# Performance work log

Measured on AMD Instinct MI355X. Metric: run time of the kernel, lower is better.

## Reference

```python
import jax, jax.numpy as jnp
import numpy as np

N_PRED, N_DRIFT, N_DW, N_NODES = 12, 2, 3, 4096
B = 128
L = N_PRED + 2 * N_DRIFT  # 16


def setup_inputs() -> dict:
    key = jax.random.key(0)
    ks = jax.random.split(key, 8)
    inp = jax.random.normal(ks[0], (B, N_NODES, N_DW, L), jnp.float32)
    ctrl = jax.random.normal(ks[1], (B, N_NODES, N_PRED), jnp.float32)
    # learned offsets (init zeros in torch; randomized here so interpolation is non-trivial)
    offset_t = jax.random.normal(ks[2], (N_DW, N_PRED), jnp.float32) * 0.5
    offset_n = jax.random.normal(ks[3], (N_DW, N_PRED), jnp.float32) * 0.5
    conv_t_w = jax.random.normal(ks[4], (1, N_DW, 3), jnp.float32) / np.sqrt(N_DW * 3)
    conv_t_b = jnp.zeros((1,), jnp.float32)
    conv_n_w = jax.random.normal(ks[5], (N_PRED, N_PRED, N_DW), jnp.float32) / np.sqrt(N_PRED * N_DW)
    conv_n_b = jnp.zeros((N_PRED,), jnp.float32)
    W = jax.random.normal(ks[6], (N_PRED, N_PRED), jnp.float32)
    bparam = jax.random.normal(ks[7], (N_NODES, N_PRED), jnp.float32)
    return dict(inp=inp, ctrl=ctrl, offset_t=offset_t, offset_n=offset_n,
                conv_t_w=conv_t_w, conv_t_b=conv_t_b, conv_n_w=conv_n_w,
                conv_n_b=conv_n_b, W=W, bparam=bparam)


def _deform(x, offset):
    # x: [BN, n_d_w, L]; offset: [n_d_w, n_pred]
    pos_add = (jnp.arange(N_PRED, dtype=jnp.float32) + N_DRIFT)[None, :]  # [1, n_pred]
    pos = jnp.tanh(offset) * N_DRIFT + pos_add                           # [d, p], in [j, j+2*drift)
    key_f = jnp.floor(pos)            # torch int(pos); pos >= 0 so floor == trunc
    frac = pos - key_f                # gradient flows to offset only through frac
    idx = key_f.astype(jnp.int32)     # [d, p]
    rows = jnp.arange(N_DW)[:, None]  # [d, 1]
    v0 = x[:, rows, idx]              # [BN, d, p]
    v1 = x[:, rows, idx + 1]
    return v0 * (1.0 - frac) + v1 * frac


def reference(inp, ctrl, offset_t, offset_n, conv_t_w, conv_t_b, conv_n_w, conv_n_b, W, bparam):
    b, n = inp.shape[0], inp.shape[1]
    x = inp.reshape(b * n, N_DW, L)
    # the written slice [n_drift:-n_drift] is exactly the interpolated region
    dt = _deform(x, offset_t)  # [BN, n_d_w, n_pred]
    dn = _deform(x, offset_n)  # [BN, n_d_w, n_pred]
    # temporal branch: Conv1d(n_d_w -> 1, k=3, pad=1)
    pred_t = jax.lax.conv_general_dilated(
        dt, conv_t_w, window_strides=(1,), padding=[(1, 1)],
        dimension_numbers=('NCH', 'OIH', 'NCH'))
    pred_t = (pred_t + conv_t_b[None, :, None]).reshape(b, n, N_PRED)
    # node branch: Conv1d(n_pred -> n_pred, k=n_d_w) over permuted [BN, n_pred, n_d_w]
    # == full contraction: out[b,o] = sum_{c,k} w[o,c,k] * dn[b,k,c]
    pred_n = (jnp.einsum('bkc,ock->bo', dn, conv_n_w) + conv_n_b).reshape(b, n, N_PRED)
    gate = jax.nn.sigmoid(jnp.einsum('bnp,pq->bnq', ctrl, W) + bparam)
    return pred_n * gate + pred_t * (1.0 - gate)
```

## Files before the change

### kernel.cpp

```cpp
#include <hip/hip_runtime.h>
#include <math.h>

#define N_PRED  12
#define N_DRIFT 2
#define N_DW    3
#define N_NODES 4096
#define BB      128
#define LL      16
#define BN      (BB * N_NODES)

__global__ void deform_precompute(const float* __restrict__ offset_t,
                                  const float* __restrict__ offset_n,
                                  const float* __restrict__ conv_t_w,
                                  const float* __restrict__ conv_n_w,
                                  float* __restrict__ Mt,
                                  float* __restrict__ Mn) {
    int t = threadIdx.x;
    if (t >= N_PRED * N_DW * LL) return;
    int q  = t % N_PRED;
    int kl = t / N_PRED;
    int k  = kl / LL;
    int l  = kl % LL;

    auto coef = [&](const float* off, int c) -> float {
        float pos = tanhf(off[k * N_PRED + c]) * (float)N_DRIFT
                    + (float)(c + N_DRIFT);
        float idf = floorf(pos);
        float fr  = pos - idf;
        int   id  = (int)idf;
        if (l == id)     return 1.0f - fr;
        if (l == id + 1) return fr;
        return 0.0f;
    };

    float mt = 0.0f;
    #pragma unroll
    for (int h = 0; h < 3; ++h) {
        int c = q - 1 + h;
        if (c < 0 || c >= N_PRED) continue;
        mt += conv_t_w[k * 3 + h] * coef(offset_t, c);
    }

    float mn = 0.0f;
    #pragma unroll
    for (int c = 0; c < N_PRED; ++c) {
        mn += conv_n_w[q * (N_PRED * N_DW) + c * N_DW + k] * coef(offset_n, c);
    }

    Mt[kl * N_PRED + q] = mt;
    Mn[kl * N_PRED + q] = mn;
}

__global__ __launch_bounds__(256) void deform_main(
        const float* __restrict__ inp,
        const float* __restrict__ ctrl,
        const float* __restrict__ W,
        const float* __restrict__ bparam,
        const float* __restrict__ conv_t_b,
        const float* __restrict__ conv_n_b,
        const float* __restrict__ Mt,
        const float* __restrict__ Mn,
        float* __restrict__ out) {
    int tid = blockIdx.x * 256 + threadIdx.x;
    int n   = tid & (N_NODES - 1);

    float x[48];
    const float4* xp = (const float4*)(inp + (size_t)tid * 48);
    #pragma unroll
    for (int i = 0; i < 12; ++i) {
        float4 v = xp[i];
        x[4 * i + 0] = v.x; x[4 * i + 1] = v.y;
        x[4 * i + 2] = v.z; x[4 * i + 3] = v.w;
    }

    float c[12];
    const float4* cp = (const float4*)(ctrl + (size_t)tid * N_PRED);
    #pragma unroll
    for (int i = 0; i < 3; ++i) {
        float4 v = cp[i];
        c[4 * i + 0] = v.x; c[4 * i + 1] = v.y;
        c[4 * i + 2] = v.z; c[4 * i + 3] = v.w;
    }

    float accg[12];
    const float4* bp = (const float4*)(bparam + (size_t)n * N_PRED);
    #pragma unroll
    for (int i = 0; i < 3; ++i) {
        float4 v = bp[i];
        accg[4 * i + 0] = v.x; accg[4 * i + 1] = v.y;
        accg[4 * i + 2] = v.z; accg[4 * i + 3] = v.w;
    }

    float acct[12], accn[12];
    float ctb = conv_t_b[0];
    #pragma unroll
    for (int q = 0; q < N_PRED; ++q) {
        acct[q] = ctb;
        accn[q] = conv_n_b[q];
    }

    #pragma unroll
    for (int kl = 0; kl < 48; ++kl) {
        float xv = x[kl];
        #pragma unroll
        for (int q = 0; q < N_PRED; ++q) {
            acct[q] = fmaf(Mt[kl * N_PRED + q], xv, acct[q]);
            accn[q] = fmaf(Mn[kl * N_PRED + q], xv, accn[q]);
        }
    }

    #pragma unroll
    for (int p = 0; p < N_PRED; ++p) {
        float cv = c[p];
        #pragma unroll
        for (int q = 0; q < N_PRED; ++q) {
            accg[q] = fmaf(cv, W[p * N_PRED + q], accg[q]);
        }
    }

    float4 o4[3];
    float* ov = (float*)o4;
    #pragma unroll
    for (int q = 0; q < N_PRED; ++q) {
        float g = 1.0f / (1.0f + __expf(-accg[q]));
        ov[q] = accn[q] * g + acct[q] * (1.0f - g);
    }
    float4* op = (float4*)(out + (size_t)tid * N_PRED);
    op[0] = o4[0]; op[1] = o4[1]; op[2] = o4[2];
}

extern "C" void kernel_launch(void* const* d_in, const int* in_sizes, int n_in,
                              void* d_out, int out_size, void* d_ws, size_t ws_size,
                              hipStream_t stream) {
    const float* inp      = (const float*)d_in[0];
    const float* ctrl     = (const float*)d_in[1];
    const float* offset_t = (const float*)d_in[2];
    const float* offset_n = (const float*)d_in[3];
    const float* conv_t_w = (const float*)d_in[4];
    const float* conv_t_b = (const float*)d_in[5];
    const float* conv_n_w = (const float*)d_in[6];
    const float* conv_n_b = (const float*)d_in[7];
    const float* W        = (const float*)d_in[8];
    const float* bparam   = (const float*)d_in[9];
    float* out = (float*)d_out;

    float* Mt = (float*)d_ws;
    float* Mn = Mt + N_DW * LL * N_PRED;

    deform_precompute<<<1, 576, 0, stream>>>(offset_t, offset_n,
                                             conv_t_w, conv_n_w, Mt, Mn);
    deform_main<<<BN / 256, 256, 0, stream>>>(inp, ctrl, W, bparam,
                                              conv_t_b, conv_n_b, Mt, Mn, out);
}
```

Baseline: 203.4 us.

## Stage input, ctrl and output through shared memory for coalesced global access

Each block cooperatively loads its slice of inp and ctrl with contiguous float4 loads into LDS (inp padded to 13 float4 per row to avoid bank conflicts). Each thread then reads its own row from LDS. Outputs are written back through LDS so the global stores are contiguous. Block size drops from 256 to 128 threads. This targets strided per-thread global access, at the cost of extra LDS traffic, barriers and about 32KB of LDS per block, which may limit occupancy.

```diff
diff --git a/kernel.cpp b/kernel.cpp
--- a/kernel.cpp
+++ b/kernel.cpp
@@ -8,6 +8,9 @@
 #define BB      128
 #define LL      16
 #define BN      (BB * N_NODES)
+#define TPB     128
+#define NBLK    (BN / TPB)
+#define XROW    13
 
 __global__ void deform_precompute(const float* __restrict__ offset_t,
                                   const float* __restrict__ offset_n,
@@ -51,7 +54,7 @@
     Mn[kl * N_PRED + q] = mn;
 }
 
-__global__ __launch_bounds__(256) void deform_main(
+__global__ __launch_bounds__(TPB) void deform_main(
         const float* __restrict__ inp,
         const float* __restrict__ ctrl,
         const float* __restrict__ W,
@@ -61,34 +64,52 @@
         const float* __restrict__ Mt,
         const float* __restrict__ Mn,
         float* __restrict__ out) {
-    int tid = blockIdx.x * 256 + threadIdx.x;
-    int n   = tid & (N_NODES - 1);
+    __shared__ float4 xs4[TPB * XROW];
+    __shared__ float4 cs4[TPB * 3];
+
+    const int t   = threadIdx.x;
+    const int tid = blockIdx.x * TPB + t;
+    const int n   = tid & (N_NODES - 1);
+
+    const float4* gin = (const float4*)inp + (size_t)blockIdx.x * (TPB * 12);
+    #pragma unroll
+    for (int i = 0; i < 12; ++i) {
+        int A = i * TPB + t;
+        float4 v = gin[A];
+        xs4[(A / 12) * XROW + (A % 12)] = v;
+    }
+    const float4* gct = (const float4*)ctrl + (size_t)blockIdx.x * (TPB * 3);
+    #pragma unroll
+    for (int i = 0; i < 3; ++i) {
+        int A = i * TPB + t;
+        cs4[A] = gct[A];
+    }
+    __syncthreads();
 
     float x[48];
-    const float4* xp = (const float4*)(inp + (size_t)tid * 48);
     #pragma unroll
-    for (int i = 0; i < 12; ++i) {
-        float4 v = xp[i];
-        x[4 * i + 0] = v.x; x[4 * i + 1] = v.y;
-        x[4 * i + 2] = v.z; x[4 * i + 3] = v.w;
+    for (int c = 0; c < 12; ++c) {
+        float4 v = xs4[t * XROW + c];
+        x[4 * c + 0] = v.x; x[4 * c + 1] = v.y;
+        x[4 * c + 2] = v.z; x[4 * c + 3] = v.w;
     }
-
-    float c[12];
-    const float4* cp = (const float4*)(ctrl + (size_t)tid * N_PRED);
+    float cr[12];
     #pragma unroll
     for (int i = 0; i < 3; ++i) {
-        float4 v = cp[i];
-        c[4 * i + 0] = v.x; c[4 * i + 1] = v.y;
-        c[4 * i + 2] = v.z; c[4 * i + 3] = v.w;
+        float4 v = cs4[t * 3 + i];
+        cr[4 * i + 0] = v.x; cr[4 * i + 1] = v.y;
+        cr[4 * i + 2] = v.z; cr[4 * i + 3] = v.w;
     }
 
     float accg[12];
-    const float4* bp = (const float4*)(bparam + (size_t)n * N_PRED);
-    #pragma unroll
-    for (int i = 0; i < 3; ++i) {
-        float4 v = bp[i];
-        accg[4 * i + 0] = v.x; accg[4 * i + 1] = v.y;
-        accg[4 * i + 2] = v.z; accg[4 * i + 3] = v.w;
+    {
+        const float* bp = bparam + (size_t)n * N_PRED;
+        #pragma unroll
+        for (int i = 0; i < 3; ++i) {
+            float4 v = *(const float4*)(bp + 4 * i);
+            accg[4 * i + 0] = v.x; accg[4 * i + 1] = v.y;
+            accg[4 * i + 2] = v.z; accg[4 * i + 3] = v.w;
+        }
     }
 
     float acct[12], accn[12];
@@ -111,7 +132,7 @@
 
     #pragma unroll
     for (int p = 0; p < N_PRED; ++p) {
-        float cv = c[p];
+        float cv = cr[p];
         #pragma unroll
         for (int q = 0; q < N_PRED; ++q) {
             accg[q] = fmaf(cv, W[p * N_PRED + q], accg[q]);
@@ -125,8 +146,19 @@
         float g = 1.0f / (1.0f + __expf(-accg[q]));
         ov[q] = accn[q] * g + acct[q] * (1.0f - g);
     }
-    float4* op = (float4*)(out + (size_t)tid * N_PRED);
-    op[0] = o4[0]; op[1] = o4[1]; op[2] = o4[2];
+
+    __syncthreads();
+    #pragma unroll
+    for (int j = 0; j < 3; ++j) {
+        xs4[t * 3 + j] = o4[j];
+    }
+    __syncthreads();
+    float4* gout = (float4*)out + (size_t)blockIdx.x * (TPB * 3);
+    #pragma unroll
+    for (int j = 0; j < 3; ++j) {
+        int A = j * TPB + t;
+        gout[A] = xs4[A];
+    }
 }
 
 extern "C" void kernel_launch(void* const* d_in, const int* in_sizes, int n_in,
@@ -149,6 +181,6 @@
 
     deform_precompute<<<1, 576, 0, stream>>>(offset_t, offset_n,
                                              conv_t_w, conv_n_w, Mt, Mn);
-    deform_main<<<BN / 256, 256, 0, stream>>>(inp, ctrl, W, bparam,
-                                              conv_t_b, conv_n_b, Mt, Mn, out);
+    deform_main<<<NBLK, TPB, 0, stream>>>(inp, ctrl, W, bparam,
+                                          conv_t_b, conv_n_b, Mt, Mn, out);
 }
```

Result: no change. 202.7 us (-0.4%).

## Process four points per thread to reuse interleaved weight loads

Applied to the files above, without the earlier changes.

Each thread now handles four points, so every precomputed weight value loaded is applied to four inputs instead of one. The two weight tables are interleaved into one array so both branches read from the same row. Inputs are streamed in chunks of twelve to bound live registers. Holding 96 accumulators per thread raises register pressure and lowers occupancy, which may hurt latency hiding on a memory-heavy kernel.

```diff
diff --git a/kernel.cpp b/kernel.cpp
--- a/kernel.cpp
+++ b/kernel.cpp
@@ -8,13 +8,16 @@
 #define BB      128
 #define LL      16
 #define BN      (BB * N_NODES)
+#define TPB     256
+#define G       4
+#define PPB     (TPB * G)
+#define NBLK    (BN / PPB)
 
 __global__ void deform_precompute(const float* __restrict__ offset_t,
                                   const float* __restrict__ offset_n,
                                   const float* __restrict__ conv_t_w,
                                   const float* __restrict__ conv_n_w,
-                                  float* __restrict__ Mt,
-                                  float* __restrict__ Mn) {
+                                  float* __restrict__ M) {
     int t = threadIdx.x;
     if (t >= N_PRED * N_DW * LL) return;
     int q  = t % N_PRED;
@@ -47,86 +50,110 @@
         mn += conv_n_w[q * (N_PRED * N_DW) + c * N_DW + k] * coef(offset_n, c);
     }
 
-    Mt[kl * N_PRED + q] = mt;
-    Mn[kl * N_PRED + q] = mn;
+    M[kl * 24 + q]      = mt;
+    M[kl * 24 + 12 + q] = mn;
 }
 
-__global__ __launch_bounds__(256) void deform_main(
+__global__ __launch_bounds__(TPB, 2) void deform_main(
         const float* __restrict__ inp,
         const float* __restrict__ ctrl,
         const float* __restrict__ W,
         const float* __restrict__ bparam,
         const float* __restrict__ conv_t_b,
         const float* __restrict__ conv_n_b,
-        const float* __restrict__ Mt,
-        const float* __restrict__ Mn,
+        const float* __restrict__ M,
         float* __restrict__ out) {
-    int tid = blockIdx.x * 256 + threadIdx.x;
-    int n   = tid & (N_NODES - 1);
+    const int t    = threadIdx.x;
+    const int base = blockIdx.x * PPB;
 
-    float x[48];
-    const float4* xp = (const float4*)(inp + (size_t)tid * 48);
+    int p[G];
     #pragma unroll
-    for (int i = 0; i < 12; ++i) {
-        float4 v = xp[i];
-        x[4 * i + 0] = v.x; x[4 * i + 1] = v.y;
-        x[4 * i + 2] = v.z; x[4 * i + 3] = v.w;
+    for (int j = 0; j < G; ++j) p[j] = base + j * TPB + t;
+
+    float acct[G][N_PRED], accn[G][N_PRED];
+    {
+        float ctb = conv_t_b[0];
+        #pragma unroll
+        for (int q = 0; q < N_PRED; ++q) {
+            float cnb = conv_n_b[q];
+            #pragma unroll
+            for (int j = 0; j < G; ++j) {
+                acct[j][q] = ctb;
+                accn[j][q] = cnb;
+            }
+        }
     }
 
-    float c[12];
-    const float4* cp = (const float4*)(ctrl + (size_t)tid * N_PRED);
-    #pragma unroll
-    for (int i = 0; i < 3; ++i) {
-        float4 v = cp[i];
-        c[4 * i + 0] = v.x; c[4 * i + 1] = v.y;
-        c[4 * i + 2] = v.z; c[4 * i + 3] = v.w;
-    }
-
-    float accg[12];
-    const float4* bp = (const float4*)(bparam + (size_t)n * N_PRED);
-    #pragma unroll
-    for (int i = 0; i < 3; ++i) {
-        float4 v = bp[i];
-        accg[4 * i + 0] = v.x; accg[4 * i + 1] = v.y;
-        accg[4 * i + 2] = v.z; accg[4 * i + 3] = v.w;
-    }
-
-    float acct[12], accn[12];
-    float ctb = conv_t_b[0];
-    #pragma unroll
-    for (int q = 0; q < N_PRED; ++q) {
-        acct[q] = ctb;
-        accn[q] = conv_n_b[q];
-    }
-
-    #pragma unroll
-    for (int kl = 0; kl < 48; ++kl) {
-        float xv = x[kl];
+    #pragma unroll 1
+    for (int c = 0; c < 4; ++c) {
+        float4 xc[G][3];
         #pragma unroll
-        for (int q = 0; q < N_PRED; ++q) {
-            acct[q] = fmaf(Mt[kl * N_PRED + q], xv, acct[q]);
-            accn[q] = fmaf(Mn[kl * N_PRED + q], xv, accn[q]);
+        for (int j = 0; j < G; ++j) {
+            const float4* xp = (const float4*)(inp + (size_t)p[j] * 48) + c * 3;
+            #pragma unroll
+            for (int i = 0; i < 3; ++i) xc[j][i] = xp[i];
+        }
+        const float* Mc = M + c * 12 * 24;
+        #pragma unroll
+        for (int kk = 0; kk < 12; ++kk) {
+            float xv[G];
+            #pragma unroll
+            for (int j = 0; j < G; ++j)
+                xv[j] = ((const float*)xc[j])[kk];
+            #pragma unroll
+            for (int q = 0; q < N_PRED; ++q) {
+                float wt = Mc[kk * 24 + q];
+                float wn = Mc[kk * 24 + 12 + q];
+                #pragma unroll
+                for (int j = 0; j < G; ++j) {
+                    acct[j][q] = fmaf(wt, xv[j], acct[j][q]);
+                    accn[j][q] = fmaf(wn, xv[j], accn[j][q]);
+                }
+            }
         }
     }
 
     #pragma unroll
-    for (int p = 0; p < N_PRED; ++p) {
-        float cv = c[p];
+    for (int j = 0; j < G; ++j) {
+        const int n = p[j] & (N_NODES - 1);
+
+        float cr[N_PRED];
+        const float4* cp = (const float4*)(ctrl + (size_t)p[j] * N_PRED);
+        #pragma unroll
+        for (int i = 0; i < 3; ++i) {
+            float4 v = cp[i];
+            cr[4 * i + 0] = v.x; cr[4 * i + 1] = v.y;
+            cr[4 * i + 2] = v.z; cr[4 * i + 3] = v.w;
+        }
+
+        float accg[N_PRED];
+        const float4* bp = (const float4*)(bparam + (size_t)n * N_PRED);
+        #pragma unroll
+        for (int i = 0; i < 3; ++i) {
+            float4 v = bp[i];
+            accg[4 * i + 0] = v.x; accg[4 * i + 1] = v.y;
+            accg[4 * i + 2] = v.z; accg[4 * i + 3] = v.w;
+        }
+
+        #pragma unroll
+        for (int pp = 0; pp < N_PRED; ++pp) {
+            float cv = cr[pp];
+            #pragma unroll
+            for (int q = 0; q < N_PRED; ++q) {
+                accg[q] = fmaf(cv, W[pp * N_PRED + q], accg[q]);
+            }
+        }
+
+        float4 o4[3];
+        float* ov = (float*)o4;
         #pragma unroll
         for (int q = 0; q < N_PRED; ++q) {
-            accg[q] = fmaf(cv, W[p * N_PRED + q], accg[q]);
+            float g = 1.0f / (1.0f + __expf(-accg[q]));
+            ov[q] = accn[j][q] * g + acct[j][q] * (1.0f - g);
         }
+        float4* op = (float4*)(out + (size_t)p[j] * N_PRED);
+        op[0] = o4[0]; op[1] = o4[1]; op[2] = o4[2];
     }
-
-    float4 o4[3];
-    float* ov = (float*)o4;
-    #pragma unroll
-    for (int q = 0; q < N_PRED; ++q) {
-        float g = 1.0f / (1.0f + __expf(-accg[q]));
-        ov[q] = accn[q] * g + acct[q] * (1.0f - g);
-    }
-    float4* op = (float4*)(out + (size_t)tid * N_PRED);
-    op[0] = o4[0]; op[1] = o4[1]; op[2] = o4[2];
 }
 
 extern "C" void kernel_launch(void* const* d_in, const int* in_sizes, int n_in,
@@ -144,11 +171,10 @@
     const float* bparam   = (const float*)d_in[9];
     float* out = (float*)d_out;
 
-    float* Mt = (float*)d_ws;
-    float* Mn = Mt + N_DW * LL * N_PRED;
+    float* M = (float*)d_ws;
 
     deform_precompute<<<1, 576, 0, stream>>>(offset_t, offset_n,
-                                             conv_t_w, conv_n_w, Mt, Mn);
-    deform_main<<<BN / 256, 256, 0, stream>>>(inp, ctrl, W, bparam,
-                                              conv_t_b, conv_n_b, Mt, Mn, out);
+                                             conv_t_w, conv_n_w, M);
+    deform_main<<<NBLK, TPB, 0, stream>>>(inp, ctrl, W, bparam,
+                                          conv_t_b, conv_n_b, M, out);
 }
```

New measurement: 225.9 us. +11.1%, slower.

## Fold all linear maps into one bf16x3 MFMA GEMM with packed weights

Applied to the files above, without the earlier changes.

Packs the deform/conv matrices, gate weight W and biases into a single 64x48 matrix, split into bf16 hi/lo parts in a precompute kernel. The main kernel then computes temporal, node and gate pre-activations with split-bf16 16x16x32 MFMA instructions per 16-row tile, replacing per-thread scalar FMA loops. This removes the scalar FMA cost and changes memory access to lane-cooperative row loads. It trades this for conversion work, masked scalar stores and a small precision loss from the three-term bf16 split.

```diff
diff --git a/kernel.cpp b/kernel.cpp
--- a/kernel.cpp
+++ b/kernel.cpp
@@ -6,24 +6,37 @@
 #define N_DW    3
 #define N_NODES 4096
 #define BB      128
-#define LL      16
 #define BN      (BB * N_NODES)
+#define NTILES  (BN / 16)
+#define RPW     4
+#define WPB     4
+#define NBLK    (NTILES / (RPW * WPB))
+
+typedef __attribute__((ext_vector_type(8))) short bf16x8;
+typedef __attribute__((ext_vector_type(4))) float f32x4;
+
+static __device__ __forceinline__ unsigned short bf16_rne(float f) {
+    unsigned int u = __float_as_uint(f);
+    u = (u + 0x7FFFu + ((u >> 16) & 1u)) >> 16;
+    return (unsigned short)u;
+}
+static __device__ __forceinline__ float bf16_to_f32(unsigned short h) {
+    return __uint_as_float(((unsigned int)h) << 16);
+}
 
 __global__ void deform_precompute(const float* __restrict__ offset_t,
                                   const float* __restrict__ offset_n,
                                   const float* __restrict__ conv_t_w,
+                                  const float* __restrict__ conv_t_b,
                                   const float* __restrict__ conv_n_w,
-                                  float* __restrict__ Mt,
-                                  float* __restrict__ Mn) {
-    int t = threadIdx.x;
-    if (t >= N_PRED * N_DW * LL) return;
-    int q  = t % N_PRED;
-    int kl = t / N_PRED;
-    int k  = kl / LL;
-    int l  = kl % LL;
-
-    auto coef = [&](const float* off, int c) -> float {
-        float pos = tanhf(off[k * N_PRED + c]) * (float)N_DRIFT
+                                  const float* __restrict__ conv_n_b,
+                                  const float* __restrict__ W,
+                                  unsigned short* __restrict__ wsB) {
+    __shared__ float Ms[64][48];
+    const int t = threadIdx.x;
+
+    auto coef = [&](const float* off, int kw, int c, int l) -> float {
+        float pos = tanhf(off[kw * N_PRED + c]) * (float)N_DRIFT
                     + (float)(c + N_DRIFT);
         float idf = floorf(pos);
         float fr  = pos - idf;
@@ -33,100 +46,140 @@
         return 0.0f;
     };
 
-    float mt = 0.0f;
-    #pragma unroll
-    for (int h = 0; h < 3; ++h) {
-        int c = q - 1 + h;
-        if (c < 0 || c >= N_PRED) continue;
-        mt += conv_t_w[k * 3 + h] * coef(offset_t, c);
-    }
-
-    float mn = 0.0f;
-    #pragma unroll
-    for (int c = 0; c < N_PRED; ++c) {
-        mn += conv_n_w[q * (N_PRED * N_DW) + c * N_DW + k] * coef(offset_n, c);
-    }
-
-    Mt[kl * N_PRED + q] = mt;
-    Mn[kl * N_PRED + q] = mn;
+    for (int e = t; e < 64 * 48; e += 256) {
+        int k = e / 48, col = e % 48;
+        float v = 0.0f;
+        if (k < 48) {
+            int kw = k >> 4, l = k & 15;
+            if (col < 12) {
+                #pragma unroll
+                for (int h = 0; h < 3; ++h) {
+                    int c = col - 1 + h;
+                    if (c < 0 || c >= N_PRED) continue;
+                    v += conv_t_w[kw * 3 + h] * coef(offset_t, kw, c, l);
+                }
+            } else if (col >= 16 && col < 28) {
+                int q = col - 16;
+                for (int c = 0; c < N_PRED; ++c)
+                    v += conv_n_w[q * (N_PRED * N_DW) + c * N_DW + kw]
+                         * coef(offset_n, kw, c, l);
+            }
+        } else if (k < 60) {
+            if (col >= 32 && col < 44) v = W[(k - 48) * N_PRED + (col - 32)];
+        } else if (k == 60) {
+            if (col < 12)                 v = conv_t_b[0];
+            else if (col >= 16 && col < 28) v = conv_n_b[col - 16];
+        }
+        Ms[k][col] = v;
+    }
+    __syncthreads();
+
+    for (int e = t; e < 3 * 2 * 64 * 8; e += 256) {
+        int j    = e & 7;
+        int lane = (e >> 3) & 63;
+        int kh   = (e >> 9) & 1;
+        int ct   = e >> 10;
+        int k    = kh * 32 + ((lane >> 4) << 3) + j;
+        int col  = (lane & 15) + 16 * ct;
+        float v  = Ms[k][col];
+        unsigned short hi = bf16_rne(v);
+        unsigned short lo = bf16_rne(v - bf16_to_f32(hi));
+        int off_hi = ((ct * 2 + kh) * 2) * 512 + lane * 8 + j;
+        wsB[off_hi]       = hi;
+        wsB[off_hi + 512] = lo;
+    }
 }
 
 __global__ __launch_bounds__(256) void deform_main(
         const float* __restrict__ inp,
         const float* __restrict__ ctrl,
-        const float* __restrict__ W,
         const float* __restrict__ bparam,
-        const float* __restrict__ conv_t_b,
-        const float* __restrict__ conv_n_b,
-        const float* __restrict__ Mt,
-        const float* __restrict__ Mn,
+        const unsigned short* __restrict__ wsB,
         float* __restrict__ out) {
-    int tid = blockIdx.x * 256 + threadIdx.x;
-    int n   = tid & (N_NODES - 1);
-
-    float x[48];
-    const float4* xp = (const float4*)(inp + (size_t)tid * 48);
+    const int lane = threadIdx.x & 63;
+    const int wid  = blockIdx.x * WPB + (threadIdx.x >> 6);
+    const int quad = lane >> 4;
+    const int col  = lane & 15;
+
+    bf16x8 Bh[3][2], Bl[3][2];
     #pragma unroll
-    for (int i = 0; i < 12; ++i) {
-        float4 v = xp[i];
-        x[4 * i + 0] = v.x; x[4 * i + 1] = v.y;
-        x[4 * i + 2] = v.z; x[4 * i + 3] = v.w;
-    }
-
-    float c[12];
-    const float4* cp = (const float4*)(ctrl + (size_t)tid * N_PRED);
-    #pragma unroll
-    for (int i = 0; i < 3; ++i) {
-        float4 v = cp[i];
-        c[4 * i + 0] = v.x; c[4 * i + 1] = v.y;
-        c[4 * i + 2] = v.z; c[4 * i + 3] = v.w;
-    }
-
-    float accg[12];
-    const float4* bp = (const float4*)(bparam + (size_t)n * N_PRED);
-    #pragma unroll
-    for (int i = 0; i < 3; ++i) {
-        float4 v = bp[i];
-        accg[4 * i + 0] = v.x; accg[4 * i + 1] = v.y;
-        accg[4 * i + 2] = v.z; accg[4 * i + 3] = v.w;
-    }
-
-    float acct[12], accn[12];
-    float ctb = conv_t_b[0];
-    #pragma unroll
-    for (int q = 0; q < N_PRED; ++q) {
-        acct[q] = ctb;
-        accn[q] = conv_n_b[q];
-    }
-
-    #pragma unroll
-    for (int kl = 0; kl < 48; ++kl) {
-        float xv = x[kl];
+    for (int ct = 0; ct < 3; ++ct) {
         #pragma unroll
-        for (int q = 0; q < N_PRED; ++q) {
-            acct[q] = fmaf(Mt[kl * N_PRED + q], xv, acct[q]);
-            accn[q] = fmaf(Mn[kl * N_PRED + q], xv, accn[q]);
-        }
-    }
-
-    #pragma unroll
-    for (int p = 0; p < N_PRED; ++p) {
-        float cv = c[p];
+        for (int kh = 0; kh < 2; ++kh) {
+            const bf16x8* ph =
+                (const bf16x8*)(wsB + ((ct * 2 + kh) * 2) * 512);
+            Bh[ct][kh] = ph[lane];
+            Bl[ct][kh] = ph[lane + 64];
+        }
+    }
+
+    const bool active = (col < 12);
+    const int  bcol   = active ? col : 11;
+
+    #pragma unroll 1
+    for (int r = 0; r < RPW; ++r) {
+        const int rt        = wid * RPW + r;
+        const int base_pair = rt * 16;
+        const int pair      = base_pair + col;
+
+        const float4* xp =
+            (const float4*)(inp + (size_t)pair * 48 + quad * 8);
+        float4 a0 = xp[0], a1 = xp[1];
+
+        const float* bbase;
+        if (quad < 2)      bbase = inp  + (size_t)pair * 48 + 32 + quad * 8;
+        else if (quad == 2) bbase = ctrl + (size_t)pair * 12;
+        else               bbase = ctrl + (size_t)pair * 12 + 8;
+        float4 b0 = *(const float4*)bbase;
+        float4 b1;
+        if (quad == 3) b1 = make_float4(1.0f, 0.0f, 0.0f, 0.0f);
+        else           b1 = *((const float4*)bbase + 1);
+
+        float za[8] = {a0.x, a0.y, a0.z, a0.w, a1.x, a1.y, a1.z, a1.w};
+        float zb[8] = {b0.x, b0.y, b0.z, b0.w, b1.x, b1.y, b1.z, b1.w};
+        union { bf16x8 v; unsigned short u[8]; } Ah0, Al0, Ah1, Al1;
         #pragma unroll
-        for (int q = 0; q < N_PRED; ++q) {
-            accg[q] = fmaf(cv, W[p * N_PRED + q], accg[q]);
-        }
-    }
-
-    float4 o4[3];
-    float* ov = (float*)o4;
-    #pragma unroll
-    for (int q = 0; q < N_PRED; ++q) {
-        float g = 1.0f / (1.0f + __expf(-accg[q]));
-        ov[q] = accn[q] * g + acct[q] * (1.0f - g);
-    }
-    float4* op = (float4*)(out + (size_t)tid * N_PRED);
-    op[0] = o4[0]; op[1] = o4[1]; op[2] = o4[2];
+        for (int j = 0; j < 8; ++j) {
+            unsigned short h0 = bf16_rne(za[j]);
+            Ah0.u[j] = h0;
+            Al0.u[j] = bf16_rne(za[j] - bf16_to_f32(h0));
+            unsigned short h1 = bf16_rne(zb[j]);
+            Ah1.u[j] = h1;
+            Al1.u[j] = bf16_rne(zb[j] - bf16_to_f32(h1));
+        }
+
+        f32x4 C0 = {0.f, 0.f, 0.f, 0.f}, C1 = C0, C2 = C0;
+        C0 = __builtin_amdgcn_mfma_f32_16x16x32_bf16(Ah0.v, Bh[0][0], C0, 0, 0, 0);
+        C0 = __builtin_amdgcn_mfma_f32_16x16x32_bf16(Ah1.v, Bh[0][1], C0, 0, 0, 0);
+        C0 = __builtin_amdgcn_mfma_f32_16x16x32_bf16(Ah0.v, Bl[0][0], C0, 0, 0, 0);
+        C0 = __builtin_amdgcn_mfma_f32_16x16x32_bf16(Ah1.v, Bl[0][1], C0, 0, 0, 0);
+        C0 = __builtin_amdgcn_mfma_f32_16x16x32_bf16(Al0.v, Bh[0][0], C0, 0, 0, 0);
+        C0 = __builtin_amdgcn_mfma_f32_16x16x32_bf16(Al1.v, Bh[0][1], C0, 0, 0, 0);
+
+        C1 = __builtin_amdgcn_mfma_f32_16x16x32_bf16(Ah0.v, Bh[1][0], C1, 0, 0, 0);
+        C1 = __builtin_amdgcn_mfma_f32_16x16x32_bf16(Ah1.v, Bh[1][1], C1, 0, 0, 0);
+        C1 = __builtin_amdgcn_mfma_f32_16x16x32_bf16(Ah0.v, Bl[1][0], C1, 0, 0, 0);
+        C1 = __builtin_amdgcn_mfma_f32_16x16x32_bf16(Ah1.v, Bl[1][1], C1, 0, 0, 0);
+        C1 = __builtin_amdgcn_mfma_f32_16x16x32_bf16(Al0.v, Bh[1][0], C1, 0, 0, 0);
+        C1 = __builtin_amdgcn_mfma_f32_16x16x32_bf16(Al1.v, Bh[1][1], C1, 0, 0, 0);
+
+        C2 = __builtin_amdgcn_mfma_f32_16x16x32_bf16(Ah0.v, Bh[2][0], C2, 0, 0, 0);
+        C2 = __builtin_amdgcn_mfma_f32_16x16x32_bf16(Ah1.v, Bh[2][1], C2, 0, 0, 0);
+        C2 = __builtin_amdgcn_mfma_f32_16x16x32_bf16(Ah0.v, Bl[2][0], C2, 0, 0, 0);
+        C2 = __builtin_amdgcn_mfma_f32_16x16x32_bf16(Ah1.v, Bl[2][1], C2, 0, 0, 0);
+        C2 = __builtin_amdgcn_mfma_f32_16x16x32_bf16(Al0.v, Bh[2][0], C2, 0, 0, 0);
+        C2 = __builtin_amdgcn_mfma_f32_16x16x32_bf16(Al1.v, Bh[2][1], C2, 0, 0, 0);
+
+        #pragma unroll
+        for (int i = 0; i < 4; ++i) {
+            int prow = base_pair + quad * 4 + i;
+            int n    = prow & (N_NODES - 1);
+            float bp = bparam[n * N_PRED + bcol];
+            float g  = 1.0f / (1.0f + __expf(-(C2[i] + bp)));
+            float o  = C1[i] * g + C0[i] * (1.0f - g);
+            if (active) out[(size_t)prow * N_PRED + col] = o;
+        }
+    }
 }
 
 extern "C" void kernel_launch(void* const* d_in, const int* in_sizes, int n_in,
@@ -144,11 +197,10 @@
     const float* bparam   = (const float*)d_in[9];
     float* out = (float*)d_out;
 
-    float* Mt = (float*)d_ws;
-    float* Mn = Mt + N_DW * LL * N_PRED;
-
-    deform_precompute<<<1, 576, 0, stream>>>(offset_t, offset_n,
-                                             conv_t_w, conv_n_w, Mt, Mn);
-    deform_main<<<BN / 256, 256, 0, stream>>>(inp, ctrl, W, bparam,
-                                              conv_t_b, conv_n_b, Mt, Mn, out);
-}
+    unsigned short* wsB = (unsigned short*)d_ws;
+
+    deform_precompute<<<1, 256, 0, stream>>>(offset_t, offset_n,
+                                             conv_t_w, conv_t_b,
+                                             conv_n_w, conv_n_b, W, wsB);
+    deform_main<<<NBLK, 256, 0, stream>>>(inp, ctrl, bparam, wsB, out);
+}
```

Result: slower. 219.6 us (+8.0%).
